# Performance work log

Hardware: AMD Instinct MI355X
Metric: run time of the kernel (lower is better)

The kernel has to match this reference:

```python
import jax, jax.numpy as jnp
import numpy as np

IN_C, HID, L, NN, BS, OUT = 32, 128, 4, 64, 512, 3
N = NN * BS  # total graph vertices
EPS_LN = 1e-5
EPS_SM = 1e-16  # PyG softmax eps


def setup_inputs() -> dict:
    key = jax.random.key(0)
    ks = jax.random.split(key, 16)
    E = 524288
    x = jax.random.normal(ks[0], (N, IN_C), dtype=jnp.float32)
    edge_index = jax.random.randint(ks[1], (2, E), 0, N, dtype=jnp.int64)
    s = 0.1
    # first GAT layer (in -> hidden)
    W0 = jax.random.normal(ks[2], (IN_C, HID), dtype=jnp.float32) * s
    att_src0 = jax.random.normal(ks[3], (HID,), dtype=jnp.float32) * s
    att_dst0 = jax.random.normal(ks[4], (HID,), dtype=jnp.float32) * s
    bias0 = jnp.zeros((HID,), dtype=jnp.float32)
    # residual GAT layers (hidden -> hidden), stacked over L
    W_res = jax.random.normal(ks[5], (L, HID, HID), dtype=jnp.float32) * s
    att_src_res = jax.random.normal(ks[6], (L, HID), dtype=jnp.float32) * s
    att_dst_res = jax.random.normal(ks[7], (L, HID), dtype=jnp.float32) * s
    bias_res = jnp.zeros((L, HID), dtype=jnp.float32)
    gamma = jnp.ones((L, HID), dtype=jnp.float32)
    beta = jnp.zeros((L, HID), dtype=jnp.float32)
    # per-node predictor heads
    W1p = jax.random.normal(ks[8], (NN, HID, HID // 2), dtype=jnp.float32) * s
    W2p = jax.random.normal(ks[9], (NN, HID // 2, OUT), dtype=jnp.float32) * s
    return {"x": x, "edge_index": edge_index, "W0": W0, "att_src0": att_src0,
            "att_dst0": att_dst0, "bias0": bias0, "W_res": W_res,
            "att_src_res": att_src_res, "att_dst_res": att_dst_res,
            "bias_res": bias_res, "gamma": gamma, "beta": beta,
            "W1p": W1p, "W2p": W2p}


def _gat(x, src, dst, W, a_src, a_dst, b):
    # PyG GATConv, heads=1, negative_slope=0.2, self-loops already appended
    h = x @ W                                   # [N, H]
    a_s = (h * a_src).sum(-1)                   # [N]
    a_d = (h * a_dst).sum(-1)                   # [N]
    e = jax.nn.leaky_relu(a_s[src] + a_d[dst], 0.2)   # [E]
    m = jax.ops.segment_max(e, dst, num_segments=N)
    e = jnp.exp(e - m[dst])
    z = jax.ops.segment_sum(e, dst, num_segments=N)
    alpha = e / (z[dst] + EPS_SM)               # [E]
    out = jax.ops.segment_sum(h[src] * alpha[:, None], dst, num_segments=N)
    return out + b


def _layernorm(x, g, b):
    mu = x.mean(-1, keepdims=True)
    var = ((x - mu) ** 2).mean(-1, keepdims=True)
    return (x - mu) * jax.lax.rsqrt(var + EPS_LN) * g + b


def reference(x, edge_index, W0, att_src0, att_dst0, bias0, W_res,
              att_src_res, att_dst_res, bias_res, gamma, beta, W1p, W2p):
    loops = jnp.arange(N, dtype=edge_index.dtype)
    src = jnp.concatenate([edge_index[0], loops])
    dst = jnp.concatenate([edge_index[1], loops])
    # first GAT + relu
    h = jax.nn.relu(_gat(x, src, dst, W0, att_src0, att_dst0, bias0))
    # res+ blocks: h = h + conv(dropout(act(norm(h))))  (dropout=identity, eval)
    for i in range(L):
        t = jax.nn.relu(_layernorm(h, gamma[i], beta[i]))
        t = _gat(t, src, dst, W_res[i], att_src_res[i], att_dst_res[i], bias_res[i])
        h = h + t
    h = jax.nn.relu(_layernorm(h, gamma[0], beta[0]))
    # per-node predictor heads
    h = h.reshape(NN, BS, HID)
    t = jax.nn.relu(jnp.einsum('nbh,nhk->nbk', h, W1p))
    logits = jnp.einsum('nbk,nko->nbo', t, W2p)
    return jax.nn.softmax(logits, axis=-1)   # softmax over class dim (dim=1 per node slice)
```

## Files before the change

### kernel.cpp

```cpp
#include <hip/hip_runtime.h>
#include <hip/hip_fp8.h>
#include <math.h>

#define NND   32768
#define HIDD  128
#define NHEAD 64
#define BSS   512
#define OUTC  3

typedef _Float16 half_t;
typedef __attribute__((ext_vector_type(8))) _Float16 half8;
typedef __attribute__((ext_vector_type(4))) float f32x4;

__device__ __forceinline__ unsigned enc_fp8x4(float a, float b, float c, float d) {
    __hip_fp8x4_e4m3 q(make_float4(a, b, c, d));
    return (unsigned)q.__x;
}
__device__ __forceinline__ float4 dec_fp8x4(unsigned v) {
    __hip_fp8x4_e4m3 t; t.__x = (__hip_fp8x4_storage_t)v;
    return (float4)t;
}

__global__ __launch_bounds__(256) void prep_kernel(const float* __restrict__ W0,
        const float* __restrict__ W_res, const float* __restrict__ W1p,
        const float* __restrict__ as0, const float* __restrict__ ad0,
        const float* __restrict__ as_res, const float* __restrict__ ad_res,
        const float* __restrict__ x, const int* __restrict__ ei, int E,
        half_t* __restrict__ Wh, half_t* __restrict__ W1h, half_t* __restrict__ W0t,
        float* __restrict__ wvec, half_t* __restrict__ xh,
        int* __restrict__ counts, int* __restrict__ rank) {
    int b = blockIdx.x, tid = threadIdx.x;
    if (b < 64) {
        __shared__ float tile[32][33];
        int l = b >> 4, t = b & 15;
        int k0 = (t >> 2) * 32, n0 = (t & 3) * 32;
        const float* src = W_res + (size_t)l * 128 * 128;
        half_t* dst = Wh + (size_t)l * 128 * 128;
        int c = tid & 31, r0 = tid >> 5;
#pragma unroll
        for (int i = 0; i < 4; ++i) tile[r0 + i * 8][c] = src[(size_t)(k0 + r0 + i * 8) * 128 + n0 + c];
        __syncthreads();
#pragma unroll
        for (int i = 0; i < 4; ++i) dst[(size_t)(n0 + r0 + i * 8) * 128 + k0 + c] = (half_t)tile[c][r0 + i * 8];
    } else if (b < 576) {
        __shared__ float tile[32][33];
        int bb = b - 64, head = bb >> 3, t = bb & 7;
        int k0 = (t >> 1) * 32, n0 = (t & 1) * 32;
        const float* src = W1p + (size_t)head * 128 * 64;
        half_t* dst = W1h + (size_t)head * 64 * 128;
        int c = tid & 31, r0 = tid >> 5;
#pragma unroll
        for (int i = 0; i < 4; ++i) tile[r0 + i * 8][c] = src[(size_t)(k0 + r0 + i * 8) * 64 + n0 + c];
        __syncthreads();
#pragma unroll
        for (int i = 0; i < 4; ++i) dst[(size_t)(n0 + r0 + i * 8) * 128 + k0 + c] = (half_t)tile[c][r0 + i * 8];
    } else if (b == 576) {
        __shared__ float t0[32][129];
        for (int i = tid; i < 4096; i += 256) t0[i >> 7][i & 127] = W0[i];
        __syncthreads();
        for (int i = tid; i < 4096; i += 256) { int n = i >> 5, k = i & 31; W0t[n * 32 + k] = (half_t)t0[k][n]; }
    } else if (b == 577) {
        for (int task = tid; task < 1088; task += 256) {
            const float* row; const float* att; int slot, sd;
            if (task < 64) {
                int k = task >> 1; sd = task & 1;
                row = W0 + k * 128; att = sd ? ad0 : as0; slot = k;
            } else {
                int tt = task - 64; int l = 1 + tt / 256; int r = tt % 256;
                int k = r >> 1; sd = r & 1;
                row = W_res + (size_t)(l - 1) * 16384 + k * 128;
                att = (sd ? ad_res : as_res) + (l - 1) * 128;
                slot = l * 128 + k;
            }
            float s = 0.f;
            for (int n = 0; n < 128; ++n) s += row[n] * att[n];
            (sd ? wvec + 640 : wvec)[slot] = s;
        }
    } else if (b < 1090) {
        int b2 = b - 578;
        const float* xs = x + (size_t)b2 * 64 * 32;
        half_t* xd = xh + (size_t)b2 * 64 * 32;
        for (int i = tid; i < 1024; i += 256) {
            float2 v = ((const float2*)xs)[i];
            union { unsigned u; half_t h[2]; } cv;
            cv.h[0] = (half_t)v.x; cv.h[1] = (half_t)v.y;
            ((unsigned*)xd)[i] = cv.u;
        }
    } else {
        int j = (b - 1090) * 256 + tid;
        int Etot = E + NND;
        if (j >= Etot) return;
        int dst = (j < E) ? ei[E + j] : (j - E);
        rank[j] = atomicAdd(&counts[dst], 1);
    }
}

__global__ __launch_bounds__(1024) void scan_kernel(const int* __restrict__ counts,
                                                    int* __restrict__ off) {
    __shared__ int sums[1024];
    int tid = threadIdx.x;
    int base = tid * 32;
    int tmp[32];
    int run = 0;
#pragma unroll
    for (int i = 0; i < 8; ++i) {
        int4 c4 = *(const int4*)&counts[base + i * 4];
        tmp[i*4+0] = run; run += c4.x;
        tmp[i*4+1] = run; run += c4.y;
        tmp[i*4+2] = run; run += c4.z;
        tmp[i*4+3] = run; run += c4.w;
    }
    sums[tid] = run;
    __syncthreads();
    for (int d = 1; d < 1024; d <<= 1) {
        int v = (tid >= d) ? sums[tid - d] : 0;
        __syncthreads();
        sums[tid] += v;
        __syncthreads();
    }
    int ebase = (tid == 0) ? 0 : sums[tid - 1];
#pragma unroll
    for (int i = 0; i < 32; ++i) off[base + i] = ebase + tmp[i];
    if (tid == 1023) off[NND] = sums[1023];
}

__global__ __launch_bounds__(256) void fill_a0_kernel(const int* __restrict__ ei, int E, int egrid,
        const int* __restrict__ off, const int* __restrict__ rank, int* __restrict__ csr_src,
        const half_t* __restrict__ xh, const float* __restrict__ wvec,
        float* __restrict__ a_s, float* __restrict__ a_d) {
    int b = blockIdx.x, tid = threadIdx.x;
    if (b < egrid) {
        int j = b * 256 + tid;
        int Etot = E + NND;
        if (j >= Etot) return;
        int src, dst;
        if (j < E) { src = ei[j]; dst = ei[E + j]; }
        else       { src = j - E; dst = j - E; }
        csr_src[off[dst] + rank[j]] = src;
    } else {
        __shared__ float ws0[32], wd0[32];
        if (tid < 32) { ws0[tid] = wvec[tid]; wd0[tid] = wvec[640 + tid]; }
        __syncthreads();
        int g = (b - egrid) * 256 + tid;
        int node = g >> 2, part = g & 3;
        half8 xv = *(const half8*)&xh[(size_t)node * 32 + part * 8];
        float s = 0.f, d2 = 0.f;
#pragma unroll
        for (int j = 0; j < 8; ++j) { float f = (float)xv[j]; s += f * ws0[part * 8 + j]; d2 += f * wd0[part * 8 + j]; }
        s += __shfl_xor(s, 1); s += __shfl_xor(s, 2);
        d2 += __shfl_xor(d2, 1); d2 += __shfl_xor(d2, 2);
        if (part == 0) { a_s[node] = s; a_d[node] = d2; }
    }
}

__global__ __launch_bounds__(1024, 4) void layer0_kernel(const half_t* __restrict__ xh,
        const float* __restrict__ asv, const float* __restrict__ adval,
        const int* __restrict__ csr_src, const int* __restrict__ off,
        const half_t* __restrict__ W0t, const float* __restrict__ bias,
        half_t* __restrict__ Hh,
        const float* __restrict__ gamma, const float* __restrict__ beta,
        unsigned char* __restrict__ Th8o,
        const float* __restrict__ wsn, const float* __restrict__ wdn,
        float* __restrict__ aso, float* __restrict__ ado) {
    __shared__ __align__(16) char smem[32768];
    half_t* Wt = (half_t*)smem;
    half_t* Ps = (half_t*)(smem + 10240);
    float*  vv = (float*)smem;
    const int tid = threadIdx.x;
    const int w = tid >> 6, lane = tid & 63, q = lane >> 4, r15 = lane & 15;
    const int n0 = blockIdx.x * 128;
    for (int i = tid; i < 512; i += 1024) {
        int n = i >> 2, c = i & 3;
        *(int4*)&Wt[n * 40 + c * 8] = *(const int4*)&W0t[(size_t)n * 32 + c * 8];
    }
    for (int t = 0; t < 8; ++t) {
        int d = n0 + w * 8 + t;
        int beg = off[d], end = off[d + 1];
        float adv = adval[d];
        float pz = 0.f, a0 = 0.f, a1 = 0.f;
        for (int base = beg; base < end; base += 64) {
            int j = base + lane;
            int s = 0; float p = 0.f;
            if (j < end) {
                s = csr_src[j];
                float tt = asv[s] + adv;
                tt = (tt > 0.f) ? tt : 0.2f * tt;
                p = __expf(tt);
            }
            pz += p;
            int cnt = end - base; if (cnt > 64) cnt = 64;
            int full = cnt & ~15;
            int k4 = 0;
            for (; k4 < full; k4 += 16) {
                int s0 = __shfl(s, k4 + q);      float p0 = __shfl(p, k4 + q);
                int s1 = __shfl(s, k4 + 4 + q);  float p1 = __shfl(p, k4 + 4 + q);
                int s2 = __shfl(s, k4 + 8 + q);  float p2 = __shfl(p, k4 + 8 + q);
                int s3 = __shfl(s, k4 + 12 + q); float p3 = __shfl(p, k4 + 12 + q);
                union { unsigned u; half_t h[2]; } u0, u1, u2, u3;
                u0.u = *(const unsigned*)&xh[(size_t)s0 * 32 + r15 * 2];
                u1.u = *(const unsigned*)&xh[(size_t)s1 * 32 + r15 * 2];
                u2.u = *(const unsigned*)&xh[(size_t)s2 * 32 + r15 * 2];
                u3.u = *(const unsigned*)&xh[(size_t)s3 * 32 + r15 * 2];
                a0 += p0 * (float)u0.h[0] + p1 * (float)u1.h[0] + p2 * (float)u2.h[0] + p3 * (float)u3.h[0];
                a1 += p0 * (float)u0.h[1] + p1 * (float)u1.h[1] + p2 * (float)u2.h[1] + p3 * (float)u3.h[1];
            }
            for (; k4 < cnt; k4 += 4) {
                int s0 = __shfl(s, k4 + q); float p0 = __shfl(p, k4 + q);
                union { unsigned u; half_t h[2]; } u0;
                u0.u = *(const unsigned*)&xh[(size_t)s0 * 32 + r15 * 2];
                a0 += p0 * (float)u0.h[0]; a1 += p0 * (float)u0.h[1];
            }
        }
#pragma unroll
        for (int o = 32; o; o >>= 1) pz += __shfl_xor(pz, o);
        a0 += __shfl_xor(a0, 16); a0 += __shfl_xor(a0, 32);
        a1 += __shfl_xor(a1, 16); a1 += __shfl_xor(a1, 32);
        if (q == 0) {
            float inv = 1.f / (pz + 1e-16f);
            union { unsigned u; half_t h[2]; } uu;
            uu.h[0] = (half_t)(a0 * inv); uu.h[1] = (half_t)(a1 * inv);
            *(unsigned*)&Ps[(w * 8 + t) * 40 + r15 * 2] = uu.u;
        }
    }
    __syncthreads();
    const int rt = w >> 1, cb = (w & 1) * 4;
    half8 af = *(const half8*)&Ps[(rt * 16 + r15) * 40 + q * 8];
    f32x4 c4[4];
#pragma unroll
    for (int ct = 0; ct < 4; ++ct) {
        f32x4 c = {0.f, 0.f, 0.f, 0.f};
        half8 bf = *(const half8*)&Wt[((cb + ct) * 16 + r15) * 40 + q * 8];
        c = __builtin_amdgcn_mfma_f32_16x16x32_f16(af, bf, c, 0, 0, 0);
        c4[ct] = c;
    }
    __syncthreads();
    const int nl = tid >> 4, sub = tid & 15;
    float4 bi0 = *(const float4*)&bias[sub * 8],  bi1 = *(const float4*)&bias[sub * 8 + 4];
    float4 g0  = *(const float4*)&gamma[sub * 8], g1  = *(const float4*)&gamma[sub * 8 + 4];
    float4 be0 = *(const float4*)&beta[sub * 8],  be1 = *(const float4*)&beta[sub * 8 + 4];
    float4 wsa = *(const float4*)&wsn[sub * 8],   wsb = *(const float4*)&wsn[sub * 8 + 4];
    float4 wda = *(const float4*)&wdn[sub * 8],   wdb = *(const float4*)&wdn[sub * 8 + 4];
    float bi[8] = {bi0.x,bi0.y,bi0.z,bi0.w,bi1.x,bi1.y,bi1.z,bi1.w};
    float gg[8] = {g0.x,g0.y,g0.z,g0.w,g1.x,g1.y,g1.z,g1.w};
    float be[8] = {be0.x,be0.y,be0.z,be0.w,be1.x,be1.y,be1.z,be1.w};
    float wsr[8] = {wsa.x,wsa.y,wsa.z,wsa.w,wsb.x,wsb.y,wsb.z,wsb.w};
    float wdr[8] = {wda.x,wda.y,wda.z,wda.w,wdb.x,wdb.y,wdb.z,wdb.w};
#pragma unroll
    for (int chunk = 0; chunk < 2; ++chunk) {
        if ((rt >> 2) == chunk) {
            int rb = (rt & 3) * 16 + q * 4;
#pragma unroll
            for (int ct = 0; ct < 4; ++ct)
#pragma unroll
                for (int r = 0; r < 4; ++r)
                    vv[(rb + r) * 128 + (cb + ct) * 16 + r15] = c4[ct][r];
        }
        __syncthreads();
        int node = n0 + chunk * 64 + nl;
        float v8[8];
#pragma unroll
        for (int j = 0; j < 8; ++j) v8[j] = fmaxf(vv[nl * 128 + sub * 8 + j] + bi[j], 0.f);
        union { int4 i4; half_t h[8]; } hw;
#pragma unroll
        for (int j = 0; j < 8; ++j) hw.h[j] = (half_t)v8[j];
        *(int4*)&Hh[(size_t)node * HIDD + sub * 8] = hw.i4;
        float sum = 0.f;
#pragma unroll
        for (int j = 0; j < 8; ++j) sum += v8[j];
#pragma unroll
        for (int o = 8; o; o >>= 1) sum += __shfl_xor(sum, o);
        float mu = sum * (1.f / HIDD);
        float var = 0.f;
#pragma unroll
        for (int j = 0; j < 8; ++j) { float dx = v8[j] - mu; var += dx * dx; }
#pragma unroll
        for (int o = 8; o; o >>= 1) var += __shfl_xor(var, o);
        float rs = rsqrtf(var * (1.f / HIDD) + 1e-5f);
        float tt[8];
        float asn = 0.f, adn = 0.f;
#pragma unroll
        for (int j = 0; j < 8; ++j) {
            float t = fmaxf((v8[j] - mu) * rs * gg[j] + be[j], 0.f);
            tt[j] = t; asn += t * wsr[j]; adn += t * wdr[j];
        }
        uint2 tw;
        tw.x = enc_fp8x4(tt[0], tt[1], tt[2], tt[3]);
        tw.y = enc_fp8x4(tt[4], tt[5], tt[6], tt[7]);
        *(uint2*)&Th8o[(size_t)node * HIDD + sub * 8] = tw;
#pragma unroll
        for (int o = 8; o; o >>= 1) { asn += __shfl_xor(asn, o); adn += __shfl_xor(adn, o); }
        if (sub == 0) { aso[node] = asn; ado[node] = adn; }
        __syncthreads();
    }
}

template <bool LAST>
__global__ __launch_bounds__(1024, 4) void layer_kernel(const unsigned char* __restrict__ F8,
        const float* __restrict__ asv, const float* __restrict__ adval,
        const int* __restrict__ csr_src, const int* __restrict__ off,
        const half_t* __restrict__ Whl, const float* __restrict__ bias,
        half_t* __restrict__ Hh,
        const float* __restrict__ gamma, const float* __restrict__ beta,
        unsigned char* __restrict__ Th8o,
        const float* __restrict__ wsn, const float* __restrict__ wdn,
        float* __restrict__ aso, float* __restrict__ ado,
        const half_t* __restrict__ W1h, const float* __restrict__ W2p,
        float* __restrict__ out) {
    __shared__ __align__(16) char smem[65536];
    half_t* Wt = (half_t*)smem;
    half_t* Ps = (half_t*)(smem + 32768);
    float*  vv = (float*)smem;
    const int tid = threadIdx.x;
    const int w = tid >> 6, lane = tid & 63, q = lane >> 4, r15 = lane & 15;
    const int n0 = blockIdx.x * 128;
    for (int i = tid; i < 2048; i += 1024) {
        int n = i >> 4, c = i & 15;
        *(int4*)&Wt[n * 128 + ((c ^ (n & 15)) * 8)] = *(const int4*)&Whl[(size_t)n * 128 + c * 8];
    }
    for (int t = 0; t < 8; ++t) {
        int d = n0 + w * 8 + t;
        int beg = off[d], end = off[d + 1];
        float adv = adval[d];
        float pz = 0.f;
        float acc[8] = {0.f,0.f,0.f,0.f,0.f,0.f,0.f,0.f};
        for (int base = beg; base < end; base += 64) {
            int j = base + lane;
            int s = 0; float p = 0.f;
            if (j < end) {
                s = csr_src[j];
                float tt = asv[s] + adv;
                tt = (tt > 0.f) ? tt : 0.2f * tt;
                p = __expf(tt);
            }
            pz += p;
            int cnt = end - base; if (cnt > 64) cnt = 64;
            int full = cnt & ~15;
            int k4 = 0;
            for (; k4 < full; k4 += 16) {
                int s0 = __shfl(s, k4 + q);      float p0 = __shfl(p, k4 + q);
                int s1 = __shfl(s, k4 + 4 + q);  float p1 = __shfl(p, k4 + 4 + q);
                int s2 = __shfl(s, k4 + 8 + q);  float p2 = __shfl(p, k4 + 8 + q);
                int s3 = __shfl(s, k4 + 12 + q); float p3 = __shfl(p, k4 + 12 + q);
                uint2 r0 = *(const uint2*)&F8[(size_t)s0 * HIDD + r15 * 8];
                uint2 r1 = *(const uint2*)&F8[(size_t)s1 * HIDD + r15 * 8];
                uint2 r2 = *(const uint2*)&F8[(size_t)s2 * HIDD + r15 * 8];
                uint2 r3 = *(const uint2*)&F8[(size_t)s3 * HIDD + r15 * 8];
                float4 f;
                f = dec_fp8x4(r0.x); acc[0]+=p0*f.x; acc[1]+=p0*f.y; acc[2]+=p0*f.z; acc[3]+=p0*f.w;
                f = dec_fp8x4(r0.y); acc[4]+=p0*f.x; acc[5]+=p0*f.y; acc[6]+=p0*f.z; acc[7]+=p0*f.w;
                f = dec_fp8x4(r1.x); acc[0]+=p1*f.x; acc[1]+=p1*f.y; acc[2]+=p1*f.z; acc[3]+=p1*f.w;
                f = dec_fp8x4(r1.y); acc[4]+=p1*f.x; acc[5]+=p1*f.y; acc[6]+=p1*f.z; acc[7]+=p1*f.w;
                f = dec_fp8x4(r2.x); acc[0]+=p2*f.x; acc[1]+=p2*f.y; acc[2]+=p2*f.z; acc[3]+=p2*f.w;
                f = dec_fp8x4(r2.y); acc[4]+=p2*f.x; acc[5]+=p2*f.y; acc[6]+=p2*f.z; acc[7]+=p2*f.w;
                f = dec_fp8x4(r3.x); acc[0]+=p3*f.x; acc[1]+=p3*f.y; acc[2]+=p3*f.z; acc[3]+=p3*f.w;
                f = dec_fp8x4(r3.y); acc[4]+=p3*f.x; acc[5]+=p3*f.y; acc[6]+=p3*f.z; acc[7]+=p3*f.w;
            }
            for (; k4 < cnt; k4 += 4) {
                int s0 = __shfl(s, k4 + q); float p0 = __shfl(p, k4 + q);
                uint2 r0 = *(const uint2*)&F8[(size_t)s0 * HIDD + r15 * 8];
                float4 f;
                f = dec_fp8x4(r0.x); acc[0]+=p0*f.x; acc[1]+=p0*f.y; acc[2]+=p0*f.z; acc[3]+=p0*f.w;
                f = dec_fp8x4(r0.y); acc[4]+=p0*f.x; acc[5]+=p0*f.y; acc[6]+=p0*f.z; acc[7]+=p0*f.w;
            }
        }
#pragma unroll
        for (int o = 32; o; o >>= 1) pz += __shfl_xor(pz, o);
#pragma unroll
        for (int i = 0; i < 8; ++i) {
            acc[i] += __shfl_xor(acc[i], 16);
            acc[i] += __shfl_xor(acc[i], 32);
        }
        if (q == 0) {
            float inv = 1.f / (pz + 1e-16f);
            union { int4 v; half_t hh[8]; } u;
#pragma unroll
            for (int i = 0; i < 8; ++i) u.hh[i] = (half_t)(acc[i] * inv);
            int m = w * 8 + t;
            *(int4*)&Ps[m * 128 + ((r15 ^ (m & 15)) * 8)] = u.v;
        }
    }
    __syncthreads();
    const int rt = w >> 1, cb = (w & 1) * 4;
    half8 af[4];
#pragma unroll
    for (int s = 0; s < 4; ++s) {
        int n = rt * 16 + r15, idx = s * 4 + q;
        af[s] = *(const half8*)&Ps[n * 128 + ((idx ^ (n & 15)) * 8)];
    }
    f32x4 c4[4];
#pragma unroll
    for (int ct = 0; ct < 4; ++ct) {
        f32x4 c = {0.f, 0.f, 0.f, 0.f};
        int n = (cb + ct) * 16 + r15;
#pragma unroll
        for (int s = 0; s < 4; ++s) {
            int idx = s * 4 + q;
            half8 bf = *(const half8*)&Wt[n * 128 + ((idx ^ (n & 15)) * 8)];
            c = __builtin_amdgcn_mfma_f32_16x16x32_f16(af[s], bf, c, 0, 0, 0);
        }
        c4[ct] = c;
    }
    __syncthreads();
    const int nl = tid >> 4, sub = tid & 15;
    float4 bi0 = *(const float4*)&bias[sub * 8],  bi1 = *(const float4*)&bias[sub * 8 + 4];
    float4 g0  = *(const float4*)&gamma[sub * 8], g1  = *(const float4*)&gamma[sub * 8 + 4];
    float4 be0 = *(const float4*)&beta[sub * 8],  be1 = *(const float4*)&beta[sub * 8 + 4];
    float bi[8] = {bi0.x,bi0.y,bi0.z,bi0.w,bi1.x,bi1.y,bi1.z,bi1.w};
    float gg[8] = {g0.x,g0.y,g0.z,g0.w,g1.x,g1.y,g1.z,g1.w};
    float be[8] = {be0.x,be0.y,be0.z,be0.w,be1.x,be1.y,be1.z,be1.w};
#pragma unroll
    for (int chunk = 0; chunk < 2; ++chunk) {
        if ((rt >> 2) == chunk) {
            int rb = (rt & 3) * 16 + q * 4;
#pragma unroll
            for (int ct = 0; ct < 4; ++ct)
#pragma unroll
                for (int r = 0; r < 4; ++r)
                    vv[(rb + r) * 128 + (cb + ct) * 16 + r15] = c4[ct][r];
        }
        __syncthreads();
        int node = n0 + chunk * 64 + nl;
        float v8[8];
        half8 hold = *(const half8*)&Hh[(size_t)node * HIDD + sub * 8];
#pragma unroll
        for (int j = 0; j < 8; ++j) v8[j] = vv[nl * 128 + sub * 8 + j] + bi[j] + (float)hold[j];
        if (!LAST) {
            union { int4 i4; half_t h[8]; } hw;
#pragma unroll
            for (int j = 0; j < 8; ++j) hw.h[j] = (half_t)v8[j];
            *(int4*)&Hh[(size_t)node * HIDD + sub * 8] = hw.i4;
        }
        float sum = 0.f;
#pragma unroll
        for (int j = 0; j < 8; ++j) sum += v8[j];
#pragma unroll
        for (int o = 8; o; o >>= 1) sum += __shfl_xor(sum, o);
        float mu = sum * (1.f / HIDD);
        float var = 0.f;
#pragma unroll
        for (int j = 0; j < 8; ++j) { float dx = v8[j] - mu; var += dx * dx; }
#pragma unroll
        for (int o = 8; o; o >>= 1) var += __shfl_xor(var, o);
        float rs = rsqrtf(var * (1.f / HIDD) + 1e-5f);
        if (!LAST) {
            float4 wsa = *(const float4*)&wsn[sub * 8], wsb = *(const float4*)&wsn[sub * 8 + 4];
            float4 wda = *(const float4*)&wdn[sub * 8], wdb = *(const float4*)&wdn[sub * 8 + 4];
            float wsr[8] = {wsa.x,wsa.y,wsa.z,wsa.w,wsb.x,wsb.y,wsb.z,wsb.w};
            float wdr[8] = {wda.x,wda.y,wda.z,wda.w,wdb.x,wdb.y,wdb.z,wdb.w};
            float tt[8];
            float asn = 0.f, adn = 0.f;
#pragma unroll
            for (int j = 0; j < 8; ++j) {
                float t = fmaxf((v8[j] - mu) * rs * gg[j] + be[j], 0.f);
                tt[j] = t; asn += t * wsr[j]; adn += t * wdr[j];
            }
            uint2 tw;
            tw.x = enc_fp8x4(tt[0], tt[1], tt[2], tt[3]);
            tw.y = enc_fp8x4(tt[4], tt[5], tt[6], tt[7]);
            *(uint2*)&Th8o[(size_t)node * HIDD + sub * 8] = tw;
#pragma unroll
            for (int o = 8; o; o >>= 1) { asn += __shfl_xor(asn, o); adn += __shfl_xor(adn, o); }
            if (sub == 0) { aso[node] = asn; ado[node] = adn; }
        } else {
            union { int4 i4; half_t h[8]; } twr;
#pragma unroll
            for (int j = 0; j < 8; ++j)
                twr.h[j] = (half_t)fmaxf((v8[j] - mu) * rs * gg[j] + be[j], 0.f);
            int g = chunk * 64 + nl;
            *(int4*)&Ps[g * 128 + ((sub ^ (g & 15)) * 8)] = twr.i4;
        }
        __syncthreads();
    }
    if (LAST) {
        if (w < 8) {
            int head = n0 >> 9;
            const half_t* W1g = W1h + (size_t)head * 64 * 128;
            half8 pa[4];
#pragma unroll
            for (int s = 0; s < 4; ++s) {
                int n = w * 16 + r15, idx = s * 4 + q;
                pa[s] = *(const half8*)&Ps[n * 128 + ((idx ^ (n & 15)) * 8)];
            }
            float lg[3][4];
#pragma unroll
            for (int o = 0; o < 3; ++o)
#pragma unroll
                for (int r = 0; r < 4; ++r) lg[o][r] = 0.f;
#pragma unroll
            for (int ct2 = 0; ct2 < 4; ++ct2) {
                int n2 = ct2 * 16 + r15;
                f32x4 c = {0.f, 0.f, 0.f, 0.f};
#pragma unroll
                for (int s = 0; s < 4; ++s) {
                    half8 bf = *(const half8*)&W1g[(size_t)n2 * 128 + s * 32 + q * 8];
                    c = __builtin_amdgcn_mfma_f32_16x16x32_f16(pa[s], bf, c, 0, 0, 0);
                }
                float w2a = W2p[(size_t)head * 192 + n2 * 3 + 0];
                float w2b = W2p[(size_t)head * 192 + n2 * 3 + 1];
                float w2c = W2p[(size_t)head * 192 + n2 * 3 + 2];
#pragma unroll
                for (int r = 0; r < 4; ++r) {
                    float t = fmaxf(c[r], 0.f);
                    lg[0][r] += t * w2a;
                    lg[1][r] += t * w2b;
                    lg[2][r] += t * w2c;
                }
            }
#pragma unroll
            for (int o = 8; o; o >>= 1)
#pragma unroll
                for (int oo = 0; oo < 3; ++oo)
#pragma unroll
                    for (int r = 0; r < 4; ++r) lg[oo][r] += __shfl_xor(lg[oo][r], o);
            if (r15 == 0) {
                int nodeD = n0 + w * 16 + q * 4;
#pragma unroll
                for (int r = 0; r < 4; ++r) {
                    float l0 = lg[0][r], l1 = lg[1][r], l2 = lg[2][r];
                    float mx = fmaxf(l0, fmaxf(l1, l2));
                    float e0 = __expf(l0 - mx), e1 = __expf(l1 - mx), e2 = __expf(l2 - mx);
                    float inv = 1.f / (e0 + e1 + e2);
                    float* op = out + (size_t)(nodeD + r) * OUTC;
                    op[0] = e0 * inv; op[1] = e1 * inv; op[2] = e2 * inv;
                }
            }
        }
    }
}

extern "C" void kernel_launch(void* const* d_in, const int* in_sizes, int n_in,
                              void* d_out, int out_size, void* d_ws, size_t ws_size,
                              hipStream_t stream) {
    const float* x        = (const float*)d_in[0];
    const int*   ei       = (const int*)d_in[1];
    const float* W0       = (const float*)d_in[2];
    const float* att_src0 = (const float*)d_in[3];
    const float* att_dst0 = (const float*)d_in[4];
    const float* bias0    = (const float*)d_in[5];
    const float* W_res    = (const float*)d_in[6];
    const float* as_res   = (const float*)d_in[7];
    const float* ad_res   = (const float*)d_in[8];
    const float* b_res    = (const float*)d_in[9];
    const float* gamma    = (const float*)d_in[10];
    const float* beta     = (const float*)d_in[11];
    const float* W1p      = (const float*)d_in[12];
    const float* W2p      = (const float*)d_in[13];
    float* out = (float*)d_out;

    int E = in_sizes[1] / 2;
    int Etot = E + NND;

    char* p = (char*)d_ws;
    auto alloc = [&](size_t bytes) { void* r = (void*)p; p += (bytes + 255) & ~(size_t)255; return r; };
    int*    counts  = (int*)alloc((size_t)NND * 4);
    int*    off     = (int*)alloc((size_t)(NND + 1) * 4);
    int*    rank    = (int*)alloc((size_t)Etot * 4);
    int*    csr_src = (int*)alloc((size_t)Etot * 4);
    half_t* xh      = (half_t*)alloc((size_t)NND * 32 * 2);
    unsigned char* Th8A = (unsigned char*)alloc((size_t)NND * HIDD);
    unsigned char* Th8B = (unsigned char*)alloc((size_t)NND * HIDD);
    half_t* Hh      = (half_t*)alloc((size_t)NND * HIDD * 2);
    float*  a_s0    = (float*)alloc((size_t)NND * 4);
    float*  a_d0    = (float*)alloc((size_t)NND * 4);
    float*  a_s1    = (float*)alloc((size_t)NND * 4);
    float*  a_d1    = (float*)alloc((size_t)NND * 4);
    half_t* Wh      = (half_t*)alloc((size_t)4 * HIDD * HIDD * 2);
    half_t* W1h     = (half_t*)alloc((size_t)NHEAD * 64 * HIDD * 2);
    half_t* W0t     = (half_t*)alloc((size_t)HIDD * 32 * 2);
    float*  wvec    = (float*)alloc((size_t)1280 * 4);

    int egrid = (Etot + 255) / 256;

    hipMemsetAsync(counts, 0, (size_t)NND * 4, stream);
    prep_kernel<<<1090 + egrid, 256, 0, stream>>>(W0, W_res, W1p, att_src0, att_dst0,
        as_res, ad_res, x, ei, E, Wh, W1h, W0t, wvec, xh, counts, rank);
    scan_kernel<<<1, 1024, 0, stream>>>(counts, off);
    fill_a0_kernel<<<egrid + 512, 256, 0, stream>>>(ei, E, egrid, off, rank, csr_src,
                                                    xh, wvec, a_s0, a_d0);

    layer0_kernel<<<256, 1024, 0, stream>>>(xh, a_s0, a_d0, csr_src, off, W0t, bias0, Hh,
        gamma, beta, Th8A, wvec + 128, wvec + 640 + 128, a_s1, a_d1);

    layer_kernel<false><<<256, 1024, 0, stream>>>(Th8A, a_s1, a_d1, csr_src, off,
        Wh, b_res, Hh, gamma + HIDD, beta + HIDD, Th8B,
        wvec + 2 * 128, wvec + 640 + 2 * 128, a_s0, a_d0, nullptr, nullptr, nullptr);
    layer_kernel<false><<<256, 1024, 0, stream>>>(Th8B, a_s0, a_d0, csr_src, off,
        Wh + 16384, b_res + HIDD, Hh, gamma + 2 * HIDD, beta + 2 * HIDD, Th8A,
        wvec + 3 * 128, wvec + 640 + 3 * 128, a_s1, a_d1, nullptr, nullptr, nullptr);
    layer_kernel<false><<<256, 1024, 0, stream>>>(Th8A, a_s1, a_d1, csr_src, off,
        Wh + 2 * 16384, b_res + 2 * HIDD, Hh, gamma + 3 * HIDD, beta + 3 * HIDD, Th8B,
        wvec + 4 * 128, wvec + 640 + 4 * 128, a_s0, a_d0, nullptr, nullptr, nullptr);

    layer_kernel<true><<<256, 1024, 0, stream>>>(Th8B, a_s0, a_d0, csr_src, off,
        Wh + 3 * 16384, b_res + 3 * HIDD, Hh, gamma, beta, nullptr,
        nullptr, nullptr, nullptr, nullptr, W1h, W2p, out);
}
```

Baseline: 288.2 us.

## Fuse all GAT layers into one persistent kernel with software grid barriers

```diff
diff --git a/kernel.cpp b/kernel.cpp
--- a/kernel.cpp
+++ b/kernel.cpp
@@ -7,6 +7,7 @@
 #define NHEAD 64
 #define BSS   512
 #define OUTC  3
+#define NBLK  256
 
 typedef _Float16 half_t;
 typedef __attribute__((ext_vector_type(8))) _Float16 half8;
@@ -19,6 +20,24 @@
 __device__ __forceinline__ float4 dec_fp8x4(unsigned v) {
     __hip_fp8x4_e4m3 t; t.__x = (__hip_fp8x4_storage_t)v;
     return (float4)t;
+}
+
+__device__ __forceinline__ void gridsync(int* cnt, int* gen) {
+    __syncthreads();
+    if (threadIdx.x == 0) {
+        __threadfence();
+        int my = __hip_atomic_load(gen, __ATOMIC_ACQUIRE, __HIP_MEMORY_SCOPE_AGENT);
+        int old = __hip_atomic_fetch_add(cnt, 1, __ATOMIC_ACQ_REL, __HIP_MEMORY_SCOPE_AGENT);
+        if (old == NBLK - 1) {
+            __hip_atomic_store(cnt, 0, __ATOMIC_RELAXED, __HIP_MEMORY_SCOPE_AGENT);
+            __hip_atomic_store(gen, my + 1, __ATOMIC_RELEASE, __HIP_MEMORY_SCOPE_AGENT);
+        } else {
+            while (__hip_atomic_load(gen, __ATOMIC_ACQUIRE, __HIP_MEMORY_SCOPE_AGENT) == my)
+                __builtin_amdgcn_s_sleep(2);
+        }
+        __threadfence();
+    }
+    __syncthreads();
 }
 
 __global__ __launch_bounds__(256) void prep_kernel(const float* __restrict__ W0,
@@ -153,43 +172,47 @@
     }
 }
 
-__global__ __launch_bounds__(1024, 4) void layer0_kernel(const half_t* __restrict__ xh,
-        const float* __restrict__ asv, const float* __restrict__ adval,
+__global__ __launch_bounds__(1024, 4) void layers_kernel(
+        const half_t* __restrict__ xh,
         const int* __restrict__ csr_src, const int* __restrict__ off,
-        const half_t* __restrict__ W0t, const float* __restrict__ bias,
-        half_t* __restrict__ Hh,
+        const half_t* __restrict__ W0t, const half_t* __restrict__ Wh,
+        const float* __restrict__ bias0, const float* __restrict__ b_res,
         const float* __restrict__ gamma, const float* __restrict__ beta,
-        unsigned char* __restrict__ Th8o,
-        const float* __restrict__ wsn, const float* __restrict__ wdn,
-        float* __restrict__ aso, float* __restrict__ ado) {
-    __shared__ __align__(16) char smem[32768];
+        const float* __restrict__ wvec,
+        half_t* __restrict__ Pbuf, half_t* __restrict__ Hh,
+        unsigned char* __restrict__ Th8A, unsigned char* __restrict__ Th8B,
+        float* __restrict__ as0, float* __restrict__ ad0,
+        float* __restrict__ as1, float* __restrict__ ad1,
+        const half_t* __restrict__ W1h, const float* __restrict__ W2p,
+        float* __restrict__ out, int* __restrict__ bar) {
+    __shared__ __align__(16) char smem[65536];
     half_t* Wt = (half_t*)smem;
-    half_t* Ps = (half_t*)(smem + 10240);
+    half_t* Ps = (half_t*)(smem + 32768);
+    half_t* Ps40 = (half_t*)(smem + 16384);
     float*  vv = (float*)smem;
+    int* cnt = bar; int* gen = bar + 1;
     const int tid = threadIdx.x;
     const int w = tid >> 6, lane = tid & 63, q = lane >> 4, r15 = lane & 15;
+    const int gw = blockIdx.x * 16 + w;
     const int n0 = blockIdx.x * 128;
-    for (int i = tid; i < 512; i += 1024) {
-        int n = i >> 2, c = i & 3;
-        *(int4*)&Wt[n * 40 + c * 8] = *(const int4*)&W0t[(size_t)n * 32 + c * 8];
-    }
-    for (int t = 0; t < 8; ++t) {
-        int d = n0 + w * 8 + t;
+    const int nl = tid >> 4, sub = tid & 15;
+
+    for (int d = gw; d < NND; d += NBLK * 16) {
         int beg = off[d], end = off[d + 1];
-        float adv = adval[d];
+        float adv = ad0[d];
         float pz = 0.f, a0 = 0.f, a1 = 0.f;
         for (int base = beg; base < end; base += 64) {
             int j = base + lane;
             int s = 0; float p = 0.f;
             if (j < end) {
                 s = csr_src[j];
-                float tt = asv[s] + adv;
+                float tt = as0[s] + adv;
                 tt = (tt > 0.f) ? tt : 0.2f * tt;
                 p = __expf(tt);
             }
             pz += p;
-            int cnt = end - base; if (cnt > 64) cnt = 64;
-            int full = cnt & ~15;
+            int cntc = end - base; if (cntc > 64) cntc = 64;
+            int full = cntc & ~15;
             int k4 = 0;
             for (; k4 < full; k4 += 16) {
                 int s0 = __shfl(s, k4 + q);      float p0 = __shfl(p, k4 + q);
@@ -204,7 +227,7 @@
                 a0 += p0 * (float)u0.h[0] + p1 * (float)u1.h[0] + p2 * (float)u2.h[0] + p3 * (float)u3.h[0];
                 a1 += p0 * (float)u0.h[1] + p1 * (float)u1.h[1] + p2 * (float)u2.h[1] + p3 * (float)u3.h[1];
             }
-            for (; k4 < cnt; k4 += 4) {
+            for (; k4 < cntc; k4 += 4) {
                 int s0 = __shfl(s, k4 + q); float p0 = __shfl(p, k4 + q);
                 union { unsigned u; half_t h[2]; } u0;
                 u0.u = *(const unsigned*)&xh[(size_t)s0 * 32 + r15 * 2];
@@ -219,310 +242,301 @@
             float inv = 1.f / (pz + 1e-16f);
             union { unsigned u; half_t h[2]; } uu;
             uu.h[0] = (half_t)(a0 * inv); uu.h[1] = (half_t)(a1 * inv);
-            *(unsigned*)&Ps[(w * 8 + t) * 40 + r15 * 2] = uu.u;
-        }
-    }
-    __syncthreads();
-    const int rt = w >> 1, cb = (w & 1) * 4;
-    half8 af = *(const half8*)&Ps[(rt * 16 + r15) * 40 + q * 8];
-    f32x4 c4[4];
-#pragma unroll
-    for (int ct = 0; ct < 4; ++ct) {
-        f32x4 c = {0.f, 0.f, 0.f, 0.f};
-        half8 bf = *(const half8*)&Wt[((cb + ct) * 16 + r15) * 40 + q * 8];
-        c = __builtin_amdgcn_mfma_f32_16x16x32_f16(af, bf, c, 0, 0, 0);
-        c4[ct] = c;
-    }
-    __syncthreads();
-    const int nl = tid >> 4, sub = tid & 15;
-    float4 bi0 = *(const float4*)&bias[sub * 8],  bi1 = *(const float4*)&bias[sub * 8 + 4];
-    float4 g0  = *(const float4*)&gamma[sub * 8], g1  = *(const float4*)&gamma[sub * 8 + 4];
-    float4 be0 = *(const float4*)&beta[sub * 8],  be1 = *(const float4*)&beta[sub * 8 + 4];
-    float4 wsa = *(const float4*)&wsn[sub * 8],   wsb = *(const float4*)&wsn[sub * 8 + 4];
-    float4 wda = *(const float4*)&wdn[sub * 8],   wdb = *(const float4*)&wdn[sub * 8 + 4];
-    float bi[8] = {bi0.x,bi0.y,bi0.z,bi0.w,bi1.x,bi1.y,bi1.z,bi1.w};
-    float gg[8] = {g0.x,g0.y,g0.z,g0.w,g1.x,g1.y,g1.z,g1.w};
-    float be[8] = {be0.x,be0.y,be0.z,be0.w,be1.x,be1.y,be1.z,be1.w};
-    float wsr[8] = {wsa.x,wsa.y,wsa.z,wsa.w,wsb.x,wsb.y,wsb.z,wsb.w};
-    float wdr[8] = {wda.x,wda.y,wda.z,wda.w,wdb.x,wdb.y,wdb.z,wdb.w};
-#pragma unroll
-    for (int chunk = 0; chunk < 2; ++chunk) {
-        if ((rt >> 2) == chunk) {
-            int rb = (rt & 3) * 16 + q * 4;
-#pragma unroll
-            for (int ct = 0; ct < 4; ++ct)
-#pragma unroll
-                for (int r = 0; r < 4; ++r)
-                    vv[(rb + r) * 128 + (cb + ct) * 16 + r15] = c4[ct][r];
-        }
-        __syncthreads();
-        int node = n0 + chunk * 64 + nl;
-        float v8[8];
-#pragma unroll
-        for (int j = 0; j < 8; ++j) v8[j] = fmaxf(vv[nl * 128 + sub * 8 + j] + bi[j], 0.f);
-        union { int4 i4; half_t h[8]; } hw;
-#pragma unroll
-        for (int j = 0; j < 8; ++j) hw.h[j] = (half_t)v8[j];
-        *(int4*)&Hh[(size_t)node * HIDD + sub * 8] = hw.i4;
-        float sum = 0.f;
-#pragma unroll
-        for (int j = 0; j < 8; ++j) sum += v8[j];
-#pragma unroll
-        for (int o = 8; o; o >>= 1) sum += __shfl_xor(sum, o);
-        float mu = sum * (1.f / HIDD);
-        float var = 0.f;
-#pragma unroll
-        for (int j = 0; j < 8; ++j) { float dx = v8[j] - mu; var += dx * dx; }
-#pragma unroll
-        for (int o = 8; o; o >>= 1) var += __shfl_xor(var, o);
-        float rs = rsqrtf(var * (1.f / HIDD) + 1e-5f);
-        float tt[8];
-        float asn = 0.f, adn = 0.f;
-#pragma unroll
-        for (int j = 0; j < 8; ++j) {
-            float t = fmaxf((v8[j] - mu) * rs * gg[j] + be[j], 0.f);
-            tt[j] = t; asn += t * wsr[j]; adn += t * wdr[j];
-        }
-        uint2 tw;
-        tw.x = enc_fp8x4(tt[0], tt[1], tt[2], tt[3]);
-        tw.y = enc_fp8x4(tt[4], tt[5], tt[6], tt[7]);
-        *(uint2*)&Th8o[(size_t)node * HIDD + sub * 8] = tw;
-#pragma unroll
-        for (int o = 8; o; o >>= 1) { asn += __shfl_xor(asn, o); adn += __shfl_xor(adn, o); }
-        if (sub == 0) { aso[node] = asn; ado[node] = adn; }
-        __syncthreads();
-    }
-}
-
-template <bool LAST>
-__global__ __launch_bounds__(1024, 4) void layer_kernel(const unsigned char* __restrict__ F8,
-        const float* __restrict__ asv, const float* __restrict__ adval,
-        const int* __restrict__ csr_src, const int* __restrict__ off,
-        const half_t* __restrict__ Whl, const float* __restrict__ bias,
-        half_t* __restrict__ Hh,
-        const float* __restrict__ gamma, const float* __restrict__ beta,
-        unsigned char* __restrict__ Th8o,
-        const float* __restrict__ wsn, const float* __restrict__ wdn,
-        float* __restrict__ aso, float* __restrict__ ado,
-        const half_t* __restrict__ W1h, const float* __restrict__ W2p,
-        float* __restrict__ out) {
-    __shared__ __align__(16) char smem[65536];
-    half_t* Wt = (half_t*)smem;
-    half_t* Ps = (half_t*)(smem + 32768);
-    float*  vv = (float*)smem;
-    const int tid = threadIdx.x;
-    const int w = tid >> 6, lane = tid & 63, q = lane >> 4, r15 = lane & 15;
-    const int n0 = blockIdx.x * 128;
-    for (int i = tid; i < 2048; i += 1024) {
-        int n = i >> 4, c = i & 15;
-        *(int4*)&Wt[n * 128 + ((c ^ (n & 15)) * 8)] = *(const int4*)&Whl[(size_t)n * 128 + c * 8];
-    }
-    for (int t = 0; t < 8; ++t) {
-        int d = n0 + w * 8 + t;
-        int beg = off[d], end = off[d + 1];
-        float adv = adval[d];
-        float pz = 0.f;
-        float acc[8] = {0.f,0.f,0.f,0.f,0.f,0.f,0.f,0.f};
-        for (int base = beg; base < end; base += 64) {
-            int j = base + lane;
-            int s = 0; float p = 0.f;
-            if (j < end) {
-                s = csr_src[j];
-                float tt = asv[s] + adv;
-                tt = (tt > 0.f) ? tt : 0.2f * tt;
-                p = __expf(tt);
-            }
-            pz += p;
-            int cnt = end - base; if (cnt > 64) cnt = 64;
-            int full = cnt & ~15;
-            int k4 = 0;
-            for (; k4 < full; k4 += 16) {
-                int s0 = __shfl(s, k4 + q);      float p0 = __shfl(p, k4 + q);
-                int s1 = __shfl(s, k4 + 4 + q);  float p1 = __shfl(p, k4 + 4 + q);
-                int s2 = __shfl(s, k4 + 8 + q);  float p2 = __shfl(p, k4 + 8 + q);
-                int s3 = __shfl(s, k4 + 12 + q); float p3 = __shfl(p, k4 + 12 + q);
-                uint2 r0 = *(const uint2*)&F8[(size_t)s0 * HIDD + r15 * 8];
-                uint2 r1 = *(const uint2*)&F8[(size_t)s1 * HIDD + r15 * 8];
-                uint2 r2 = *(const uint2*)&F8[(size_t)s2 * HIDD + r15 * 8];
-                uint2 r3 = *(const uint2*)&F8[(size_t)s3 * HIDD + r15 * 8];
-                float4 f;
-                f = dec_fp8x4(r0.x); acc[0]+=p0*f.x; acc[1]+=p0*f.y; acc[2]+=p0*f.z; acc[3]+=p0*f.w;
-                f = dec_fp8x4(r0.y); acc[4]+=p0*f.x; acc[5]+=p0*f.y; acc[6]+=p0*f.z; acc[7]+=p0*f.w;
-                f = dec_fp8x4(r1.x); acc[0]+=p1*f.x; acc[1]+=p1*f.y; acc[2]+=p1*f.z; acc[3]+=p1*f.w;
-                f = dec_fp8x4(r1.y); acc[4]+=p1*f.x; acc[5]+=p1*f.y; acc[6]+=p1*f.z; acc[7]+=p1*f.w;
-                f = dec_fp8x4(r2.x); acc[0]+=p2*f.x; acc[1]+=p2*f.y; acc[2]+=p2*f.z; acc[3]+=p2*f.w;
-                f = dec_fp8x4(r2.y); acc[4]+=p2*f.x; acc[5]+=p2*f.y; acc[6]+=p2*f.z; acc[7]+=p2*f.w;
-                f = dec_fp8x4(r3.x); acc[0]+=p3*f.x; acc[1]+=p3*f.y; acc[2]+=p3*f.z; acc[3]+=p3*f.w;
-                f = dec_fp8x4(r3.y); acc[4]+=p3*f.x; acc[5]+=p3*f.y; acc[6]+=p3*f.z; acc[7]+=p3*f.w;
-            }
-            for (; k4 < cnt; k4 += 4) {
-                int s0 = __shfl(s, k4 + q); float p0 = __shfl(p, k4 + q);
-                uint2 r0 = *(const uint2*)&F8[(size_t)s0 * HIDD + r15 * 8];
-                float4 f;
-                f = dec_fp8x4(r0.x); acc[0]+=p0*f.x; acc[1]+=p0*f.y; acc[2]+=p0*f.z; acc[3]+=p0*f.w;
-                f = dec_fp8x4(r0.y); acc[4]+=p0*f.x; acc[5]+=p0*f.y; acc[6]+=p0*f.z; acc[7]+=p0*f.w;
-            }
-        }
-#pragma unroll
-        for (int o = 32; o; o >>= 1) pz += __shfl_xor(pz, o);
-#pragma unroll
-        for (int i = 0; i < 8; ++i) {
-            acc[i] += __shfl_xor(acc[i], 16);
-            acc[i] += __shfl_xor(acc[i], 32);
-        }
-        if (q == 0) {
-            float inv = 1.f / (pz + 1e-16f);
-            union { int4 v; half_t hh[8]; } u;
-#pragma unroll
-            for (int i = 0; i < 8; ++i) u.hh[i] = (half_t)(acc[i] * inv);
-            int m = w * 8 + t;
-            *(int4*)&Ps[m * 128 + ((r15 ^ (m & 15)) * 8)] = u.v;
-        }
-    }
-    __syncthreads();
-    const int rt = w >> 1, cb = (w & 1) * 4;
-    half8 af[4];
-#pragma unroll
-    for (int s = 0; s < 4; ++s) {
-        int n = rt * 16 + r15, idx = s * 4 + q;
-        af[s] = *(const half8*)&Ps[n * 128 + ((idx ^ (n & 15)) * 8)];
-    }
-    f32x4 c4[4];
-#pragma unroll
-    for (int ct = 0; ct < 4; ++ct) {
-        f32x4 c = {0.f, 0.f, 0.f, 0.f};
-        int n = (cb + ct) * 16 + r15;
-#pragma unroll
-        for (int s = 0; s < 4; ++s) {
-            int idx = s * 4 + q;
-            half8 bf = *(const half8*)&Wt[n * 128 + ((idx ^ (n & 15)) * 8)];
-            c = __builtin_amdgcn_mfma_f32_16x16x32_f16(af[s], bf, c, 0, 0, 0);
-        }
-        c4[ct] = c;
-    }
-    __syncthreads();
-    const int nl = tid >> 4, sub = tid & 15;
-    float4 bi0 = *(const float4*)&bias[sub * 8],  bi1 = *(const float4*)&bias[sub * 8 + 4];
-    float4 g0  = *(const float4*)&gamma[sub * 8], g1  = *(const float4*)&gamma[sub * 8 + 4];
-    float4 be0 = *(const float4*)&beta[sub * 8],  be1 = *(const float4*)&beta[sub * 8 + 4];
-    float bi[8] = {bi0.x,bi0.y,bi0.z,bi0.w,bi1.x,bi1.y,bi1.z,bi1.w};
-    float gg[8] = {g0.x,g0.y,g0.z,g0.w,g1.x,g1.y,g1.z,g1.w};
-    float be[8] = {be0.x,be0.y,be0.z,be0.w,be1.x,be1.y,be1.z,be1.w};
-#pragma unroll
-    for (int chunk = 0; chunk < 2; ++chunk) {
-        if ((rt >> 2) == chunk) {
-            int rb = (rt & 3) * 16 + q * 4;
-#pragma unroll
-            for (int ct = 0; ct < 4; ++ct)
-#pragma unroll
-                for (int r = 0; r < 4; ++r)
-                    vv[(rb + r) * 128 + (cb + ct) * 16 + r15] = c4[ct][r];
-        }
-        __syncthreads();
-        int node = n0 + chunk * 64 + nl;
-        float v8[8];
-        half8 hold = *(const half8*)&Hh[(size_t)node * HIDD + sub * 8];
-#pragma unroll
-        for (int j = 0; j < 8; ++j) v8[j] = vv[nl * 128 + sub * 8 + j] + bi[j] + (float)hold[j];
-        if (!LAST) {
+            *(unsigned*)&Pbuf[(size_t)d * 32 + r15 * 2] = uu.u;
+        }
+    }
+    gridsync(cnt, gen);
+
+    {
+        for (int i = tid; i < 512; i += 1024) {
+            int n = i >> 2, c = i & 3;
+            *(int4*)&Wt[n * 40 + c * 8] = *(const int4*)&W0t[(size_t)n * 32 + c * 8];
+        }
+        for (int i = tid; i < 512; i += 1024) {
+            int n = i >> 2, c = i & 3;
+            *(int4*)&Ps40[n * 40 + c * 8] = *(const int4*)&Pbuf[(size_t)(n0 + n) * 32 + c * 8];
+        }
+        __syncthreads();
+        const int rt = w >> 1, cb = (w & 1) * 4;
+        half8 af = *(const half8*)&Ps40[(rt * 16 + r15) * 40 + q * 8];
+        f32x4 c4[4];
+#pragma unroll
+        for (int ct = 0; ct < 4; ++ct) {
+            f32x4 c = {0.f, 0.f, 0.f, 0.f};
+            half8 bf = *(const half8*)&Wt[((cb + ct) * 16 + r15) * 40 + q * 8];
+            c = __builtin_amdgcn_mfma_f32_16x16x32_f16(af, bf, c, 0, 0, 0);
+            c4[ct] = c;
+        }
+        __syncthreads();
+        const float* wsn = wvec + 128;
+        const float* wdn = wvec + 640 + 128;
+#pragma unroll
+        for (int chunk = 0; chunk < 2; ++chunk) {
+            if ((rt >> 2) == chunk) {
+                int rb = (rt & 3) * 16 + q * 4;
+#pragma unroll
+                for (int ct = 0; ct < 4; ++ct)
+#pragma unroll
+                    for (int r = 0; r < 4; ++r)
+                        vv[(rb + r) * 128 + (cb + ct) * 16 + r15] = c4[ct][r];
+            }
+            __syncthreads();
+            int node = n0 + chunk * 64 + nl;
+            float v8[8];
+#pragma unroll
+            for (int j = 0; j < 8; ++j) v8[j] = fmaxf(vv[nl * 128 + sub * 8 + j] + bias0[sub * 8 + j], 0.f);
             union { int4 i4; half_t h[8]; } hw;
 #pragma unroll
             for (int j = 0; j < 8; ++j) hw.h[j] = (half_t)v8[j];
             *(int4*)&Hh[(size_t)node * HIDD + sub * 8] = hw.i4;
-        }
-        float sum = 0.f;
-#pragma unroll
-        for (int j = 0; j < 8; ++j) sum += v8[j];
-#pragma unroll
-        for (int o = 8; o; o >>= 1) sum += __shfl_xor(sum, o);
-        float mu = sum * (1.f / HIDD);
-        float var = 0.f;
-#pragma unroll
-        for (int j = 0; j < 8; ++j) { float dx = v8[j] - mu; var += dx * dx; }
-#pragma unroll
-        for (int o = 8; o; o >>= 1) var += __shfl_xor(var, o);
-        float rs = rsqrtf(var * (1.f / HIDD) + 1e-5f);
-        if (!LAST) {
-            float4 wsa = *(const float4*)&wsn[sub * 8], wsb = *(const float4*)&wsn[sub * 8 + 4];
-            float4 wda = *(const float4*)&wdn[sub * 8], wdb = *(const float4*)&wdn[sub * 8 + 4];
-            float wsr[8] = {wsa.x,wsa.y,wsa.z,wsa.w,wsb.x,wsb.y,wsb.z,wsb.w};
-            float wdr[8] = {wda.x,wda.y,wda.z,wda.w,wdb.x,wdb.y,wdb.z,wdb.w};
-            float tt[8];
-            float asn = 0.f, adn = 0.f;
+            float sum = 0.f;
+#pragma unroll
+            for (int j = 0; j < 8; ++j) sum += v8[j];
+#pragma unroll
+            for (int o = 8; o; o >>= 1) sum += __shfl_xor(sum, o);
+            float mu = sum * (1.f / HIDD);
+            float var = 0.f;
+#pragma unroll
+            for (int j = 0; j < 8; ++j) { float dx = v8[j] - mu; var += dx * dx; }
+#pragma unroll
+            for (int o = 8; o; o >>= 1) var += __shfl_xor(var, o);
+            float rs = rsqrtf(var * (1.f / HIDD) + 1e-5f);
+            float tt[8]; float asn = 0.f, adn = 0.f;
 #pragma unroll
             for (int j = 0; j < 8; ++j) {
-                float t = fmaxf((v8[j] - mu) * rs * gg[j] + be[j], 0.f);
-                tt[j] = t; asn += t * wsr[j]; adn += t * wdr[j];
+                float t = fmaxf((v8[j] - mu) * rs * gamma[sub * 8 + j] + beta[sub * 8 + j], 0.f);
+                tt[j] = t; asn += t * wsn[sub * 8 + j]; adn += t * wdn[sub * 8 + j];
             }
             uint2 tw;
             tw.x = enc_fp8x4(tt[0], tt[1], tt[2], tt[3]);
             tw.y = enc_fp8x4(tt[4], tt[5], tt[6], tt[7]);
-            *(uint2*)&Th8o[(size_t)node * HIDD + sub * 8] = tw;
+            *(uint2*)&Th8A[(size_t)node * HIDD + sub * 8] = tw;
 #pragma unroll
             for (int o = 8; o; o >>= 1) { asn += __shfl_xor(asn, o); adn += __shfl_xor(adn, o); }
-            if (sub == 0) { aso[node] = asn; ado[node] = adn; }
-        } else {
-            union { int4 i4; half_t h[8]; } twr;
-#pragma unroll
-            for (int j = 0; j < 8; ++j)
-                twr.h[j] = (half_t)fmaxf((v8[j] - mu) * rs * gg[j] + be[j], 0.f);
-            int g = chunk * 64 + nl;
-            *(int4*)&Ps[g * 128 + ((sub ^ (g & 15)) * 8)] = twr.i4;
-        }
-        __syncthreads();
-    }
-    if (LAST) {
-        if (w < 8) {
-            int head = n0 >> 9;
-            const half_t* W1g = W1h + (size_t)head * 64 * 128;
-            half8 pa[4];
+            if (sub == 0) { as1[node] = asn; ad1[node] = adn; }
+            __syncthreads();
+        }
+    }
+    gridsync(cnt, gen);
+
+    for (int L = 0; L < 4; ++L) {
+        const unsigned char* Fin = (L & 1) ? Th8B : Th8A;
+        unsigned char* Fout      = (L & 1) ? Th8A : Th8B;
+        const float* asv = (L & 1) ? as0 : as1;
+        const float* adv_ = (L & 1) ? ad0 : ad1;
+        float* aso = (L & 1) ? as1 : as0;
+        float* ado = (L & 1) ? ad1 : ad0;
+        const bool last = (L == 3);
+        const float* bia = b_res + L * HIDD;
+        const float* gam = gamma + (last ? 0 : (L + 1)) * HIDD;
+        const float* bet = beta + (last ? 0 : (L + 1)) * HIDD;
+        const float* wsn = wvec + (L + 2) * 128;
+        const float* wdn = wvec + 640 + (L + 2) * 128;
+        const half_t* Whl = Wh + (size_t)L * 16384;
+
+        for (int d = gw; d < NND; d += NBLK * 16) {
+            int beg = off[d], end = off[d + 1];
+            float adv2 = adv_[d];
+            float pz = 0.f;
+            float acc[8] = {0.f,0.f,0.f,0.f,0.f,0.f,0.f,0.f};
+            for (int base = beg; base < end; base += 64) {
+                int j = base + lane;
+                int s = 0; float p = 0.f;
+                if (j < end) {
+                    s = csr_src[j];
+                    float tt = asv[s] + adv2;
+                    tt = (tt > 0.f) ? tt : 0.2f * tt;
+                    p = __expf(tt);
+                }
+                pz += p;
+                int cntc = end - base; if (cntc > 64) cntc = 64;
+                int full = cntc & ~15;
+                int k4 = 0;
+                for (; k4 < full; k4 += 16) {
+                    int s0 = __shfl(s, k4 + q);      float p0 = __shfl(p, k4 + q);
+                    int s1 = __shfl(s, k4 + 4 + q);  float p1 = __shfl(p, k4 + 4 + q);
+                    int s2 = __shfl(s, k4 + 8 + q);  float p2 = __shfl(p, k4 + 8 + q);
+                    int s3 = __shfl(s, k4 + 12 + q); float p3 = __shfl(p, k4 + 12 + q);
+                    uint2 r0 = *(const uint2*)&Fin[(size_t)s0 * HIDD + r15 * 8];
+                    uint2 r1 = *(const uint2*)&Fin[(size_t)s1 * HIDD + r15 * 8];
+                    uint2 r2 = *(const uint2*)&Fin[(size_t)s2 * HIDD + r15 * 8];
+                    uint2 r3 = *(const uint2*)&Fin[(size_t)s3 * HIDD + r15 * 8];
+                    float4 f;
+                    f = dec_fp8x4(r0.x); acc[0]+=p0*f.x; acc[1]+=p0*f.y; acc[2]+=p0*f.z; acc[3]+=p0*f.w;
+                    f = dec_fp8x4(r0.y); acc[4]+=p0*f.x; acc[5]+=p0*f.y; acc[6]+=p0*f.z; acc[7]+=p0*f.w;
+                    f = dec_fp8x4(r1.x); acc[0]+=p1*f.x; acc[1]+=p1*f.y; acc[2]+=p1*f.z; acc[3]+=p1*f.w;
+                    f = dec_fp8x4(r1.y); acc[4]+=p1*f.x; acc[5]+=p1*f.y; acc[6]+=p1*f.z; acc[7]+=p1*f.w;
+                    f = dec_fp8x4(r2.x); acc[0]+=p2*f.x; acc[1]+=p2*f.y; acc[2]+=p2*f.z; acc[3]+=p2*f.w;
+                    f = dec_fp8x4(r2.y); acc[4]+=p2*f.x; acc[5]+=p2*f.y; acc[6]+=p2*f.z; acc[7]+=p2*f.w;
+                    f = dec_fp8x4(r3.x); acc[0]+=p3*f.x; acc[1]+=p3*f.y; acc[2]+=p3*f.z; acc[3]+=p3*f.w;
+                    f = dec_fp8x4(r3.y); acc[4]+=p3*f.x; acc[5]+=p3*f.y; acc[6]+=p3*f.z; acc[7]+=p3*f.w;
+                }
+                for (; k4 < cntc; k4 += 4) {
+                    int s0 = __shfl(s, k4 + q); float p0 = __shfl(p, k4 + q);
+                    uint2 r0 = *(const uint2*)&Fin[(size_t)s0 * HIDD + r15 * 8];
+                    float4 f;
+                    f = dec_fp8x4(r0.x); acc[0]+=p0*f.x; acc[1]+=p0*f.y; acc[2]+=p0*f.z; acc[3]+=p0*f.w;
+                    f = dec_fp8x4(r0.y); acc[4]+=p0*f.x; acc[5]+=p0*f.y; acc[6]+=p0*f.z; acc[7]+=p0*f.w;
+                }
+            }
+#pragma unroll
+            for (int o = 32; o; o >>= 1) pz += __shfl_xor(pz, o);
+#pragma unroll
+            for (int i = 0; i < 8; ++i) {
+                acc[i] += __shfl_xor(acc[i], 16);
+                acc[i] += __shfl_xor(acc[i], 32);
+            }
+            if (q == 0) {
+                float inv = 1.f / (pz + 1e-16f);
+                union { int4 v; half_t hh[8]; } u;
+#pragma unroll
+                for (int i = 0; i < 8; ++i) u.hh[i] = (half_t)(acc[i] * inv);
+                *(int4*)&Pbuf[(size_t)d * HIDD + r15 * 8] = u.v;
+            }
+        }
+        gridsync(cnt, gen);
+
+        for (int i = tid; i < 2048; i += 1024) {
+            int n = i >> 4, c = i & 15;
+            *(int4*)&Wt[n * 128 + ((c ^ (n & 15)) * 8)] = *(const int4*)&Whl[(size_t)n * 128 + c * 8];
+        }
+        for (int i = tid; i < 2048; i += 1024) {
+            int n = i >> 4, c = i & 15;
+            *(int4*)&Ps[n * 128 + ((c ^ (n & 15)) * 8)] = *(const int4*)&Pbuf[(size_t)(n0 + n) * HIDD + c * 8];
+        }
+        __syncthreads();
+        const int rt = w >> 1, cb = (w & 1) * 4;
+        half8 af[4];
+#pragma unroll
+        for (int s = 0; s < 4; ++s) {
+            int n = rt * 16 + r15, idx = s * 4 + q;
+            af[s] = *(const half8*)&Ps[n * 128 + ((idx ^ (n & 15)) * 8)];
+        }
+        f32x4 c4[4];
+#pragma unroll
+        for (int ct = 0; ct < 4; ++ct) {
+            f32x4 c = {0.f, 0.f, 0.f, 0.f};
+            int n = (cb + ct) * 16 + r15;
 #pragma unroll
             for (int s = 0; s < 4; ++s) {
-                int n = w * 16 + r15, idx = s * 4 + q;
-                pa[s] = *(const half8*)&Ps[n * 128 + ((idx ^ (n & 15)) * 8)];
-            }
-            float lg[3][4];
-#pragma unroll
-            for (int o = 0; o < 3; ++o)
-#pragma unroll
-                for (int r = 0; r < 4; ++r) lg[o][r] = 0.f;
-#pragma unroll
-            for (int ct2 = 0; ct2 < 4; ++ct2) {
-                int n2 = ct2 * 16 + r15;
-                f32x4 c = {0.f, 0.f, 0.f, 0.f};
-#pragma unroll
-                for (int s = 0; s < 4; ++s) {
-                    half8 bf = *(const half8*)&W1g[(size_t)n2 * 128 + s * 32 + q * 8];
-                    c = __builtin_amdgcn_mfma_f32_16x16x32_f16(pa[s], bf, c, 0, 0, 0);
+                int idx = s * 4 + q;
+                half8 bf = *(const half8*)&Wt[n * 128 + ((idx ^ (n & 15)) * 8)];
+                c = __builtin_amdgcn_mfma_f32_16x16x32_f16(af[s], bf, c, 0, 0, 0);
+            }
+            c4[ct] = c;
+        }
+        __syncthreads();
+#pragma unroll
+        for (int chunk = 0; chunk < 2; ++chunk) {
+            if ((rt >> 2) == chunk) {
+                int rb = (rt & 3) * 16 + q * 4;
+#pragma unroll
+                for (int ct = 0; ct < 4; ++ct)
+#pragma unroll
+                    for (int r = 0; r < 4; ++r)
+                        vv[(rb + r) * 128 + (cb + ct) * 16 + r15] = c4[ct][r];
+            }
+            __syncthreads();
+            int node = n0 + chunk * 64 + nl;
+            float v8[8];
+            half8 hold = *(const half8*)&Hh[(size_t)node * HIDD + sub * 8];
+#pragma unroll
+            for (int j = 0; j < 8; ++j) v8[j] = vv[nl * 128 + sub * 8 + j] + bia[sub * 8 + j] + (float)hold[j];
+            if (!last) {
+                union { int4 i4; half_t h[8]; } hw;
+#pragma unroll
+                for (int j = 0; j < 8; ++j) hw.h[j] = (half_t)v8[j];
+                *(int4*)&Hh[(size_t)node * HIDD + sub * 8] = hw.i4;
+            }
+            float sum = 0.f;
+#pragma unroll
+            for (int j = 0; j < 8; ++j) sum += v8[j];
+#pragma unroll
+            for (int o = 8; o; o >>= 1) sum += __shfl_xor(sum, o);
+            float mu = sum * (1.f / HIDD);
+            float var = 0.f;
+#pragma unroll
+            for (int j = 0; j < 8; ++j) { float dx = v8[j] - mu; var += dx * dx; }
+#pragma unroll
+            for (int o = 8; o; o >>= 1) var += __shfl_xor(var, o);
+            float rs = rsqrtf(var * (1.f / HIDD) + 1e-5f);
+            if (!last) {
+                float tt[8]; float asn = 0.f, adn = 0.f;
+#pragma unroll
+                for (int j = 0; j < 8; ++j) {
+                    float t = fmaxf((v8[j] - mu) * rs * gam[sub * 8 + j] + bet[sub * 8 + j], 0.f);
+                    tt[j] = t; asn += t * wsn[sub * 8 + j]; adn += t * wdn[sub * 8 + j];
                 }
-                float w2a = W2p[(size_t)head * 192 + n2 * 3 + 0];
-                float w2b = W2p[(size_t)head * 192 + n2 * 3 + 1];
-                float w2c = W2p[(size_t)head * 192 + n2 * 3 + 2];
-#pragma unroll
-                for (int r = 0; r < 4; ++r) {
-                    float t = fmaxf(c[r], 0.f);
-                    lg[0][r] += t * w2a;
-                    lg[1][r] += t * w2b;
-                    lg[2][r] += t * w2c;
-                }
-            }
-#pragma unroll
-            for (int o = 8; o; o >>= 1)
-#pragma unroll
-                for (int oo = 0; oo < 3; ++oo)
-#pragma unroll
-                    for (int r = 0; r < 4; ++r) lg[oo][r] += __shfl_xor(lg[oo][r], o);
-            if (r15 == 0) {
-                int nodeD = n0 + w * 16 + q * 4;
-#pragma unroll
-                for (int r = 0; r < 4; ++r) {
-                    float l0 = lg[0][r], l1 = lg[1][r], l2 = lg[2][r];
-                    float mx = fmaxf(l0, fmaxf(l1, l2));
-                    float e0 = __expf(l0 - mx), e1 = __expf(l1 - mx), e2 = __expf(l2 - mx);
-                    float inv = 1.f / (e0 + e1 + e2);
-                    float* op = out + (size_t)(nodeD + r) * OUTC;
-                    op[0] = e0 * inv; op[1] = e1 * inv; op[2] = e2 * inv;
-                }
+                uint2 tw;
+                tw.x = enc_fp8x4(tt[0], tt[1], tt[2], tt[3]);
+                tw.y = enc_fp8x4(tt[4], tt[5], tt[6], tt[7]);
+                *(uint2*)&Fout[(size_t)node * HIDD + sub * 8] = tw;
+#pragma unroll
+                for (int o = 8; o; o >>= 1) { asn += __shfl_xor(asn, o); adn += __shfl_xor(adn, o); }
+                if (sub == 0) { aso[node] = asn; ado[node] = adn; }
+            } else {
+                union { int4 i4; half_t h[8]; } twr;
+#pragma unroll
+                for (int j = 0; j < 8; ++j)
+                    twr.h[j] = (half_t)fmaxf((v8[j] - mu) * rs * gam[sub * 8 + j] + bet[sub * 8 + j], 0.f);
+                int g = chunk * 64 + nl;
+                *(int4*)&Ps[g * 128 + ((sub ^ (g & 15)) * 8)] = twr.i4;
+            }
+            __syncthreads();
+        }
+        if (!last) gridsync(cnt, gen);
+    }
+
+    if (w < 8) {
+        int head = n0 >> 9;
+        const half_t* W1g = W1h + (size_t)head * 64 * 128;
+        half8 pa[4];
+#pragma unroll
+        for (int s = 0; s < 4; ++s) {
+            int n = w * 16 + r15, idx = s * 4 + q;
+            pa[s] = *(const half8*)&Ps[n * 128 + ((idx ^ (n & 15)) * 8)];
+        }
+        float lg[3][4];
+#pragma unroll
+        for (int o = 0; o < 3; ++o)
+#pragma unroll
+            for (int r = 0; r < 4; ++r) lg[o][r] = 0.f;
+#pragma unroll
+        for (int ct2 = 0; ct2 < 4; ++ct2) {
+            int n2 = ct2 * 16 + r15;
+            f32x4 c = {0.f, 0.f, 0.f, 0.f};
+#pragma unroll
+            for (int s = 0; s < 4; ++s) {
+                half8 bf = *(const half8*)&W1g[(size_t)n2 * 128 + s * 32 + q * 8];
+                c = __builtin_amdgcn_mfma_f32_16x16x32_f16(pa[s], bf, c, 0, 0, 0);
+            }
+            float w2a = W2p[(size_t)head * 192 + n2 * 3 + 0];
+            float w2b = W2p[(size_t)head * 192 + n2 * 3 + 1];
+            float w2c = W2p[(size_t)head * 192 + n2 * 3 + 2];
+#pragma unroll
+            for (int r = 0; r < 4; ++r) {
+                float t = fmaxf(c[r], 0.f);
+                lg[0][r] += t * w2a;
+                lg[1][r] += t * w2b;
+                lg[2][r] += t * w2c;
+            }
+        }
+#pragma unroll
+        for (int o = 8; o; o >>= 1)
+#pragma unroll
+            for (int oo = 0; oo < 3; ++oo)
+#pragma unroll
+                for (int r = 0; r < 4; ++r) lg[oo][r] += __shfl_xor(lg[oo][r], o);
+        if (r15 == 0) {
+            int nodeD = n0 + w * 16 + q * 4;
+#pragma unroll
+            for (int r = 0; r < 4; ++r) {
+                float l0 = lg[0][r], l1 = lg[1][r], l2 = lg[2][r];
+                float mx = fmaxf(l0, fmaxf(l1, l2));
+                float e0 = __expf(l0 - mx), e1 = __expf(l1 - mx), e2 = __expf(l2 - mx);
+                float inv = 1.f / (e0 + e1 + e2);
+                float* op = out + (size_t)(nodeD + r) * OUTC;
+                op[0] = e0 * inv; op[1] = e1 * inv; op[2] = e2 * inv;
             }
         }
     }
@@ -552,11 +566,13 @@
 
     char* p = (char*)d_ws;
     auto alloc = [&](size_t bytes) { void* r = (void*)p; p += (bytes + 255) & ~(size_t)255; return r; };
+    int*    bar     = (int*)alloc(256);
     int*    counts  = (int*)alloc((size_t)NND * 4);
     int*    off     = (int*)alloc((size_t)(NND + 1) * 4);
     int*    rank    = (int*)alloc((size_t)Etot * 4);
     int*    csr_src = (int*)alloc((size_t)Etot * 4);
     half_t* xh      = (half_t*)alloc((size_t)NND * 32 * 2);
+    half_t* Pbuf    = (half_t*)alloc((size_t)NND * HIDD * 2);
     unsigned char* Th8A = (unsigned char*)alloc((size_t)NND * HIDD);
     unsigned char* Th8B = (unsigned char*)alloc((size_t)NND * HIDD);
     half_t* Hh      = (half_t*)alloc((size_t)NND * HIDD * 2);
@@ -571,27 +587,14 @@
 
     int egrid = (Etot + 255) / 256;
 
-    hipMemsetAsync(counts, 0, (size_t)NND * 4, stream);
+    hipMemsetAsync(bar, 0, 256 + (size_t)NND * 4, stream);
     prep_kernel<<<1090 + egrid, 256, 0, stream>>>(W0, W_res, W1p, att_src0, att_dst0,
         as_res, ad_res, x, ei, E, Wh, W1h, W0t, wvec, xh, counts, rank);
     scan_kernel<<<1, 1024, 0, stream>>>(counts, off);
     fill_a0_kernel<<<egrid + 512, 256, 0, stream>>>(ei, E, egrid, off, rank, csr_src,
                                                     xh, wvec, a_s0, a_d0);
 
-    layer0_kernel<<<256, 1024, 0, stream>>>(xh, a_s0, a_d0, csr_src, off, W0t, bias0, Hh,
-        gamma, beta, Th8A, wvec + 128, wvec + 640 + 128, a_s1, a_d1);
-
-    layer_kernel<false><<<256, 1024, 0, stream>>>(Th8A, a_s1, a_d1, csr_src, off,
-        Wh, b_res, Hh, gamma + HIDD, beta + HIDD, Th8B,
-        wvec + 2 * 128, wvec + 640 + 2 * 128, a_s0, a_d0, nullptr, nullptr, nullptr);
-    layer_kernel<false><<<256, 1024, 0, stream>>>(Th8B, a_s0, a_d0, csr_src, off,
-        Wh + 16384, b_res + HIDD, Hh, gamma + 2 * HIDD, beta + 2 * HIDD, Th8A,
-        wvec + 3 * 128, wvec + 640 + 3 * 128, a_s1, a_d1, nullptr, nullptr, nullptr);
-    layer_kernel<false><<<256, 1024, 0, stream>>>(Th8A, a_s1, a_d1, csr_src, off,
-        Wh + 2 * 16384, b_res + 2 * HIDD, Hh, gamma + 3 * HIDD, beta + 3 * HIDD, Th8B,
-        wvec + 4 * 128, wvec + 640 + 4 * 128, a_s0, a_d0, nullptr, nullptr, nullptr);
-
-    layer_kernel<true><<<256, 1024, 0, stream>>>(Th8B, a_s0, a_d0, csr_src, off,
-        Wh + 3 * 16384, b_res + 3 * HIDD, Hh, gamma, beta, nullptr,
-        nullptr, nullptr, nullptr, nullptr, W1h, W2p, out);
-}
+    layers_kernel<<<NBLK, 1024, 0, stream>>>(xh, csr_src, off, W0t, Wh, bias0, b_res,
+        gamma, beta, wvec, Pbuf, Hh, Th8A, Th8B,
+        a_s0, a_d0, a_s1, a_d1, W1h, W2p, out, bar);
+}
```

Result: slower. 632.2 us (+119.3%).
